# Optimization experiments

Hardware: AMD Instinct MI355X
Metric: run time of the kernel (lower is better)

Reference implementation:

```python
import jax, jax.numpy as jnp
import numpy as np

N = 500_000          # number of particles
D = 6                # phase-space dimension
N_BINS = 128         # bins per axis
SQRT2 = 1.4142135623730951
BANDWIDTH = 1.0      # kernel width relative to bin width (module default)


def setup_inputs() -> dict:
    key = jax.random.key(0)
    x = jax.random.normal(key, (N, D), dtype=jnp.float32)
    edges = jnp.linspace(-3.0, 3.0, N_BINS + 1, dtype=jnp.float32)
    return {"x": x, "bin_edges_x": edges, "bin_edges_y": edges}


def _cdf_weights(u, edges, bw):
    """Per-point Gaussian mass in each bin via CDF (erf) differences.

    u: (n,), edges: (m+1,) -> weights (n, m); row sums <= 1.
    """
    z = jax.scipy.special.erf((edges[None, :] - u[:, None]) / (bw * SQRT2))  # (n, m+1)
    return 0.5 * (z[:, 1:] - z[:, :-1])  # (n, m)


def reference(x, bin_edges_x, bin_edges_y):
    dx = bin_edges_x[1] - bin_edges_x[0]
    dy = bin_edges_y[1] - bin_edges_y[0]
    bw_x = BANDWIDTH * dx
    bw_y = BANDWIDTH * dy
    # axis = (0, 1): project onto first two phase-space coordinates
    wx = _cdf_weights(x[:, 0], bin_edges_x, bw_x)  # (n, bx)
    wy = _cdf_weights(x[:, 1], bin_edges_y, bw_y)  # (n, by)
    hist = jnp.einsum('ni,nj->ij', wx, wy)         # (bx, by)
    # normalize to a probability density over the grid
    hist = hist / (hist.sum() * dx * dy)
    return hist
```

## Files before the change

kernel.cpp:

```cpp
#include <hip/hip_runtime.h>
#include <math.h>


#define NBINS   128
#define NB2     (NBINS * NBINS)
#define KC      256
#define AX_B    32768
#define THREADS 512
#define NBLOCKS 512
#define QSCALE  320.0f

typedef int i32x4 __attribute__((ext_vector_type(4)));

static __device__ __forceinline__ unsigned short f2bf(float f) {
    unsigned int b = __float_as_uint(f);
    b += 0x7fff + ((b >> 16) & 1);
    return (unsigned short)(b >> 16);
}
static __device__ __forceinline__ float bf2f(unsigned short u) {
    return __uint_as_float((unsigned int)u << 16);
}

static __device__ __forceinline__ float erf_fast(float x) {
    const float ax = fabsf(x);
    const float t  = __builtin_amdgcn_rcpf(fmaf(0.3275911f, ax, 1.0f));
    const float e  = __expf(-x * x);
    float p = fmaf(1.061405429f, t, -1.453152027f);
    p = fmaf(p, t, 1.421413741f);
    p = fmaf(p, t, -0.284496736f);
    p = fmaf(p, t, 0.254829592f);
    p = p * t;
    return copysignf(fmaf(-p, e, 1.0f), x);
}

__global__ __launch_bounds__(THREADS, 4) void hist_mfma_kernel(
    const float* __restrict__ x,
    const float* __restrict__ edges_x,
    const float* __restrict__ edges_y,
    unsigned short* __restrict__ partials,
    float* __restrict__ btot,
    int n)
{
    __shared__ __align__(16) signed char sh[2 * AX_B];
    __shared__ int xw[8];

    const int tid  = threadIdx.x;
    const int lane = tid & 63;
    const int wv   = tid >> 6;

    const float e0x = edges_x[0];
    const float dxw = edges_x[1] - e0x;
    const float e0y = edges_y[0];
    const float dyw = edges_y[1] - e0y;

    const int axis = tid >> 8;
    const int pl   = tid & 255;
    const float e0   = axis ? e0y : e0x;
    const float invd = 1.0f / (axis ? dyw : dxw);
    const float cc   = 0.7071067811865476f;
    signed char* const sdst =
        sh + axis * AX_B + (pl >> 6) * 1024 + ((pl >> 4) & 3) * 256 + (pl & 15);

    i32x4 acc[4][4];
    #pragma unroll
    for (int i = 0; i < 4; ++i)
        #pragma unroll
        for (int j = 0; j < 4; ++j)
            acc[i][j] = (i32x4){0, 0, 0, 0};

    const int rowQ = ((wv >> 1) & 1) * 4;
    const int colQ = (wv & 1) * 4;
    const int ks0  = (wv >> 2) * 2;

    const int nchunks = (n + KC - 1) / KC;

    float u = 1e30f;
    {
        const int p = blockIdx.x * KC + pl;
        if (blockIdx.x < nchunks && p < n) u = x[(size_t)p * 6 + axis];
    }
    int b0;
    signed char qv[8];
    {
        const float spos = (u - e0) * invd;
        int b = (int)floorf(spos + 0.5f) - 4;
        b0 = b < 0 ? 0 : (b > NBINS - 8 ? NBINS - 8 : b);
        const float t0 = ((float)b0 - spos) * cc;
        float z[9];
        #pragma unroll
        for (int k = 0; k < 9; ++k) z[k] = erf_fast(t0 + (float)k * cc);
        #pragma unroll
        for (int k = 0; k < 8; ++k)
            qv[k] = (signed char)(int)rintf(0.5f * (z[k + 1] - z[k]) * QSCALE);
    }

    for (int chunk = blockIdx.x; chunk < nchunks; chunk += gridDim.x) {
        const int nchunk = chunk + gridDim.x;
        float un = 1e30f;
        if (nchunk < nchunks) {
            const int pn = nchunk * KC + pl;
            if (pn < n) un = x[(size_t)pn * 6 + axis];
        }

        float4* zp = (float4*)sh;
        #pragma unroll
        for (int i = 0; i < 8; ++i)
            zp[tid + i * THREADS] = (float4){0.f, 0.f, 0.f, 0.f};
        __syncthreads();

        #pragma unroll
        for (int k = 0; k < 8; ++k) {
            const int b = b0 + k;
            sdst[(b >> 4) * 4096 + (b & 15) * 16] = qv[k];
        }
        __syncthreads();

        #pragma unroll
        for (int s = 0; s < 2; ++s) {
            const int ks = ks0 + s;
            i32x4 av[4], bv[4];
            #pragma unroll
            for (int i = 0; i < 4; ++i)
                av[i] = *(const i32x4*)(sh + (rowQ + i) * 4096 + ks * 1024 + lane * 16);
            #pragma unroll
            for (int j = 0; j < 4; ++j)
                bv[j] = *(const i32x4*)(sh + AX_B + (colQ + j) * 4096 + ks * 1024 + lane * 16);
            #pragma unroll
            for (int i = 0; i < 4; ++i)
                #pragma unroll
                for (int j = 0; j < 4; ++j)
                    acc[i][j] = __builtin_amdgcn_mfma_i32_16x16x64_i8(
                        av[i], bv[j], acc[i][j], 0, 0, 0);
        }

        {
            const float spos = (un - e0) * invd;
            int b = (int)floorf(spos + 0.5f) - 4;
            b0 = b < 0 ? 0 : (b > NBINS - 8 ? NBINS - 8 : b);
            const float t0 = ((float)b0 - spos) * cc;
            float z[9];
            #pragma unroll
            for (int k = 0; k < 9; ++k) z[k] = erf_fast(t0 + (float)k * cc);
            #pragma unroll
            for (int k = 0; k < 8; ++k)
                qv[k] = (signed char)(int)rintf(0.5f * (z[k + 1] - z[k]) * QSCALE);
        }
        __syncthreads();
    }

    if (wv >= 4) {
        int* dst = (int*)sh + (wv - 4) * 4096;
        #pragma unroll
        for (int i = 0; i < 4; ++i)
            #pragma unroll
            for (int j = 0; j < 4; ++j)
                #pragma unroll
                for (int g = 0; g < 4; ++g)
                    dst[((i * 4 + j) * 4 + g) * 64 + lane] = acc[i][j][g];
    }
    __syncthreads();

    int bsum = 0;
    if (wv < 4) {
        const float qs = 1.0f / (QSCALE * QSCALE);
        const int* src = (const int*)sh + wv * 4096;
        unsigned short* my = partials + (size_t)blockIdx.x * NB2;
        const int r0 = (lane >> 4) * 4;
        const int c0 = lane & 15;
        #pragma unroll
        for (int i = 0; i < 4; ++i)
            #pragma unroll
            for (int j = 0; j < 4; ++j)
                #pragma unroll
                for (int g = 0; g < 4; ++g) {
                    const int v = acc[i][j][g] + src[((i * 4 + j) * 4 + g) * 64 + lane];
                    bsum += v;
                    const int row = (rowQ + i) * 16 + r0 + g;
                    const int col = (colQ + j) * 16 + c0;
                    my[row * NBINS + col] = f2bf((float)v * qs);
                }
    }
    #pragma unroll
    for (int off = 32; off > 0; off >>= 1) bsum += __shfl_down(bsum, off, 64);
    if (lane == 0) xw[wv] = bsum;
    __syncthreads();
    if (tid == 0) {
        const float qs = 1.0f / (QSCALE * QSCALE);
        btot[blockIdx.x] = (float)(xw[0] + xw[1] + xw[2] + xw[3]) * qs;
    }
}

__global__ void reduce_kernel(const unsigned short* __restrict__ partials,
                              const float* __restrict__ btot,
                              const float* __restrict__ edges_x,
                              const float* __restrict__ edges_y,
                              float* __restrict__ out)
{
    __shared__ float4 red[8][32];
    __shared__ float ws[4];
    __shared__ float stot;

    const int t = threadIdx.x;
    const int bin4 = t & 31;
    const int pg = t >> 5;
    const int binBase = blockIdx.x * 128;

    float tl = btot[t] + btot[t + 256];
    #pragma unroll
    for (int off = 32; off > 0; off >>= 1) tl += __shfl_down(tl, off, 64);
    if ((t & 63) == 0) ws[t >> 6] = tl;

    const unsigned short* p =
        partials + (size_t)(pg * 64) * NB2 + binBase + bin4 * 4;
    float4 s = {0.f, 0.f, 0.f, 0.f};
    #pragma unroll 8
    for (int k = 0; k < 64; ++k) {
        const ushort4 v = *(const ushort4*)(p + (size_t)k * NB2);
        s.x += bf2f(v.x); s.y += bf2f(v.y); s.z += bf2f(v.z); s.w += bf2f(v.w);
    }
    red[pg][bin4] = s;
    __syncthreads();

    if (t == 0) {
        const float dxw = edges_x[1] - edges_x[0];
        const float dyw = edges_y[1] - edges_y[0];
        stot = 1.0f / ((ws[0] + ws[1] + ws[2] + ws[3]) * dxw * dyw);
    }
    __syncthreads();

    if (t < 32) {
        float4 a = red[0][t];
        #pragma unroll
        for (int g = 1; g < 8; ++g) {
            const float4 b = red[g][t];
            a.x += b.x; a.y += b.y; a.z += b.z; a.w += b.w;
        }
        a.x *= stot; a.y *= stot; a.z *= stot; a.w *= stot;
        *(float4*)(out + binBase + t * 4) = a;
    }
}

extern "C" void kernel_launch(void* const* d_in, const int* in_sizes, int n_in,
                              void* d_out, int out_size, void* d_ws, size_t ws_size,
                              hipStream_t stream)
{
    const float* x  = (const float*)d_in[0];
    const float* ex = (const float*)d_in[1];
    const float* ey = (const float*)d_in[2];
    float* out = (float*)d_out;
    const int n = in_sizes[0] / 6;

    unsigned short* partials = (unsigned short*)d_ws;
    float* btot = (float*)((char*)d_ws + (size_t)NBLOCKS * NB2 * 2);

    hist_mfma_kernel<<<NBLOCKS, THREADS, 0, stream>>>(x, ex, ey, partials, btot, n);
    reduce_kernel<<<NB2 / 128, 256, 0, stream>>>(partials, btot, ex, ey, out);
}
```

Measured before the change: 86.13 us.

## Double-buffer LDS weight tiles and clear only previously written bins

Chunk size is halved and LDS is split into two ping-pong buffers, so scattering the next chunk's weights overlaps the MFMA step on the current buffer and each iteration needs one barrier instead of three. The full LDS zeroing per chunk is replaced by zeroing only the bins written two chunks earlier. Two threads now share each particle-axis pair and compute 4 erf bins each, doubling the threads per point. This costs more loop iterations and twice as many global loads of x, plus more complex bookkeeping of old bin offsets.

```diff
diff --git a/kernel.cpp b/kernel.cpp
--- a/kernel.cpp
+++ b/kernel.cpp
@@ -4,8 +4,9 @@
 
 #define NBINS   128
 #define NB2     (NBINS * NBINS)
-#define KC      256
-#define AX_B    32768
+#define KC      128
+#define AXB     16384
+#define BUFB    (2 * AXB)
 #define THREADS 512
 #define NBLOCKS 512
 #define QSCALE  320.0f
@@ -41,7 +42,7 @@
     float* __restrict__ btot,
     int n)
 {
-    __shared__ __align__(16) signed char sh[2 * AX_B];
+    __shared__ __align__(16) signed char sh[2 * BUFB];
     __shared__ int xw[8];
 
     const int tid  = threadIdx.x;
@@ -53,13 +54,14 @@
     const float e0y = edges_y[0];
     const float dyw = edges_y[1] - e0y;
 
-    const int axis = tid >> 8;
-    const int pl   = tid & 255;
-    const float e0   = axis ? e0y : e0x;
-    const float invd = 1.0f / (axis ? dyw : dxw);
+    const int a  = tid >> 8;
+    const int pl = (tid & 255) >> 1;
+    const int h  = tid & 1;
+    const float e0   = a ? e0y : e0x;
+    const float invd = 1.0f / (a ? dyw : dxw);
     const float cc   = 0.7071067811865476f;
-    signed char* const sdst =
-        sh + axis * AX_B + (pl >> 6) * 1024 + ((pl >> 4) & 3) * 256 + (pl & 15);
+    signed char* const sbase =
+        sh + a * AXB + (pl >> 6) * 1024 + ((pl >> 4) & 3) * 256 + (pl & 15);
 
     i32x4 acc[4][4];
     #pragma unroll
@@ -70,82 +72,91 @@
 
     const int rowQ = ((wv >> 1) & 1) * 4;
     const int colQ = (wv & 1) * 4;
-    const int ks0  = (wv >> 2) * 2;
+    const int ks   = wv >> 2;
+    const signed char* const rbase = sh + ks * 1024 + lane * 16;
 
     const int nchunks = (n + KC - 1) / KC;
 
-    float u = 1e30f;
-    {
-        const int p = blockIdx.x * KC + pl;
-        if (blockIdx.x < nchunks && p < n) u = x[(size_t)p * 6 + axis];
-    }
-    int b0;
-    signed char qv[8];
-    {
+    auto loadu = [&](int c) -> float {
+        if (c < nchunks) {
+            const int p = c * KC + pl;
+            if (p < n) return x[(size_t)p * 6 + a];
+        }
+        return 1e30f;
+    };
+    int b0; signed char qv[4];
+    auto calc = [&](float u) {
         const float spos = (u - e0) * invd;
         int b = (int)floorf(spos + 0.5f) - 4;
         b0 = b < 0 ? 0 : (b > NBINS - 8 ? NBINS - 8 : b);
-        const float t0 = ((float)b0 - spos) * cc;
-        float z[9];
-        #pragma unroll
-        for (int k = 0; k < 9; ++k) z[k] = erf_fast(t0 + (float)k * cc);
-        #pragma unroll
-        for (int k = 0; k < 8; ++k)
+        const float t0 = ((float)(b0 + 4 * h) - spos) * cc;
+        float z[5];
+        #pragma unroll
+        for (int k = 0; k < 5; ++k) z[k] = erf_fast(t0 + (float)k * cc);
+        #pragma unroll
+        for (int k = 0; k < 4; ++k)
             qv[k] = (signed char)(int)rintf(0.5f * (z[k + 1] - z[k]) * QSCALE);
-    }
-
-    for (int chunk = blockIdx.x; chunk < nchunks; chunk += gridDim.x) {
-        const int nchunk = chunk + gridDim.x;
-        float un = 1e30f;
-        if (nchunk < nchunks) {
-            const int pn = nchunk * KC + pl;
-            if (pn < n) un = x[(size_t)pn * 6 + axis];
-        }
-
-        float4* zp = (float4*)sh;
-        #pragma unroll
-        for (int i = 0; i < 8; ++i)
-            zp[tid + i * THREADS] = (float4){0.f, 0.f, 0.f, 0.f};
-        __syncthreads();
-
-        #pragma unroll
-        for (int k = 0; k < 8; ++k) {
-            const int b = b0 + k;
-            sdst[(b >> 4) * 4096 + (b & 15) * 16] = qv[k];
-        }
-        __syncthreads();
-
-        #pragma unroll
-        for (int s = 0; s < 2; ++s) {
-            const int ks = ks0 + s;
-            i32x4 av[4], bv[4];
-            #pragma unroll
-            for (int i = 0; i < 4; ++i)
-                av[i] = *(const i32x4*)(sh + (rowQ + i) * 4096 + ks * 1024 + lane * 16);
+    };
+    auto scat = [&](int Woff, int b0old) {
+        #pragma unroll
+        for (int k = 0; k < 4; ++k) {
+            const int b = b0old + 4 * h + k;
+            sbase[Woff + (b >> 4) * 2048 + (b & 15) * 16] = 0;
+        }
+        #pragma unroll
+        for (int k = 0; k < 4; ++k) {
+            const int b = b0 + 4 * h + k;
+            sbase[Woff + (b >> 4) * 2048 + (b & 15) * 16] = qv[k];
+        }
+    };
+    auto mstep = [&](int Roff) {
+        i32x4 av[4], bv[4];
+        #pragma unroll
+        for (int i = 0; i < 4; ++i)
+            av[i] = *(const i32x4*)(rbase + Roff + (rowQ + i) * 2048);
+        #pragma unroll
+        for (int j = 0; j < 4; ++j)
+            bv[j] = *(const i32x4*)(rbase + Roff + AXB + (colQ + j) * 2048);
+        #pragma unroll
+        for (int i = 0; i < 4; ++i)
             #pragma unroll
             for (int j = 0; j < 4; ++j)
-                bv[j] = *(const i32x4*)(sh + AX_B + (colQ + j) * 4096 + ks * 1024 + lane * 16);
-            #pragma unroll
-            for (int i = 0; i < 4; ++i)
-                #pragma unroll
-                for (int j = 0; j < 4; ++j)
-                    acc[i][j] = __builtin_amdgcn_mfma_i32_16x16x64_i8(
-                        av[i], bv[j], acc[i][j], 0, 0, 0);
-        }
-
+                acc[i][j] = __builtin_amdgcn_mfma_i32_16x16x64_i8(
+                    av[i], bv[j], acc[i][j], 0, 0, 0);
+    };
+
+    float4* zp = (float4*)sh;
+    #pragma unroll
+    for (int i = 0; i < 8; ++i)
+        zp[tid + i * THREADS] = (float4){0.f, 0.f, 0.f, 0.f};
+
+    int c = blockIdx.x;
+    float u1 = loadu(c + NBLOCKS);
+    calc(loadu(c));
+    int b0A = 0, b0B = 0;
+    __syncthreads();
+    scat(0, b0A); b0A = b0;
+    __syncthreads();
+
+    while (true) {
         {
-            const float spos = (un - e0) * invd;
-            int b = (int)floorf(spos + 0.5f) - 4;
-            b0 = b < 0 ? 0 : (b > NBINS - 8 ? NBINS - 8 : b);
-            const float t0 = ((float)b0 - spos) * cc;
-            float z[9];
-            #pragma unroll
-            for (int k = 0; k < 9; ++k) z[k] = erf_fast(t0 + (float)k * cc);
-            #pragma unroll
-            for (int k = 0; k < 8; ++k)
-                qv[k] = (signed char)(int)rintf(0.5f * (z[k + 1] - z[k]) * QSCALE);
-        }
-        __syncthreads();
+            const float u2 = loadu(c + 2 * NBLOCKS);
+            calc(u1);
+            scat(BUFB, b0B); b0B = b0;
+            mstep(0);
+            __syncthreads();
+            c += NBLOCKS; u1 = u2;
+            if (c >= nchunks) break;
+        }
+        {
+            const float u2 = loadu(c + 2 * NBLOCKS);
+            calc(u1);
+            scat(0, b0A); b0A = b0;
+            mstep(BUFB);
+            __syncthreads();
+            c += NBLOCKS; u1 = u2;
+            if (c >= nchunks) break;
+        }
     }
 
     if (wv >= 4) {
@@ -229,14 +240,14 @@
     __syncthreads();
 
     if (t < 32) {
-        float4 a = red[0][t];
+        float4 aa = red[0][t];
         #pragma unroll
         for (int g = 1; g < 8; ++g) {
             const float4 b = red[g][t];
-            a.x += b.x; a.y += b.y; a.z += b.z; a.w += b.w;
-        }
-        a.x *= stot; a.y *= stot; a.z *= stot; a.w *= stot;
-        *(float4*)(out + binBase + t * 4) = a;
+            aa.x += b.x; aa.y += b.y; aa.z += b.z; aa.w += b.w;
+        }
+        aa.x *= stot; aa.y *= stot; aa.z *= stot; aa.w *= stot;
+        *(float4*)(out + binBase + t * 4) = aa;
     }
 }
 
```

Result: no change. 86.37 us (+0.3%).
